# Performance work log

Measured on AMD Instinct MI355X. Metric: run time of the kernel, lower is better.

Reference implementation:

```python
import jax, jax.numpy as jnp
import numpy as np

CUM_P = 0.9  # cumulative_p
MIN_KEEP = 1  # min_tokens_to_keep (<=1 -> branch is a no-op, as in torch default)


def setup_inputs() -> dict:
    key = jax.random.key(0)
    k1, k2 = jax.random.split(key, 2)
    B, D, V = 64, 2048, 50257
    x = jax.random.normal(k1, (B, D), dtype=jnp.float32)
    W = jax.random.normal(k2, (D, V), dtype=jnp.float32) * (1.0 / np.sqrt(D))
    b = jnp.zeros((V,), dtype=jnp.float32)
    return {"x": x, "W": W, "b": b}


def _nucleus_probs(x, W, b):
    # proj + softmax -> probs over vocab  [B, V]
    probs = jax.nn.softmax(x @ W + b, axis=-1)
    # descending sort over vocab
    sorted_idx = jnp.argsort(-probs, axis=-1)                      # [B, V]
    sorted_p = jnp.take_along_axis(probs, sorted_idx, axis=-1)    # [B, V]
    cum = jnp.cumsum(sorted_p, axis=-1)
    remove_sorted = cum > CUM_P
    # shift right by one so the token that crosses the threshold is kept
    remove_sorted = jnp.concatenate(
        [jnp.zeros_like(remove_sorted[..., :1]), remove_sorted[..., :-1]], axis=-1
    )
    # scatter mask back to original vocab order
    rows = jnp.arange(probs.shape[0])[:, None]                     # [B, 1]
    remove = jnp.zeros_like(remove_sorted).at[rows, sorted_idx].set(remove_sorted)
    kept = jnp.where(remove, 0.0, probs)
    # renormalize exactly as torch: p * 1/(sum + 1e-6)
    return kept * (1.0 / (kept.sum(axis=-1, keepdims=True) + 1e-6))


def reference(x, W, b):
    p = _nucleus_probs(x, W, b)                                    # [B, V]
    # Categorical(probs).sample(); zeros -> log = -inf (never sampled)
    return jax.random.categorical(jax.random.key(42), jnp.log(p), axis=-1)
```

## Files before the change

kernel.cpp:

```cpp
#include <hip/hip_runtime.h>
#include <hip/hip_bf16.h>
#include <stdint.h>

#define BB 64
#define DD 2048
#define VV 50257
#define VP 50260
#define NQ 12565
#define NB 4096
#define MAXC 2048
#define QS 8
#define QCH 6283
#define SK 4

typedef __attribute__((ext_vector_type(8))) short short8;
typedef __attribute__((ext_vector_type(4))) float f32x4;
typedef float f32x4u __attribute__((vector_size(16), aligned(4)));

struct U2 { unsigned x, y; };

__device__ __forceinline__ unsigned rotl32(unsigned v, int r) {
  return (v << r) | (v >> (32 - r));
}

__device__ __forceinline__ U2 threefry2x32(unsigned k0, unsigned k1,
                                           unsigned x0, unsigned x1) {
  unsigned k2 = k0 ^ k1 ^ 0x1BD11BDAu;
  x0 += k0; x1 += k1;
#define TF_R4(r1, r2, r3, r4)                         \
  x0 += x1; x1 = rotl32(x1, r1); x1 ^= x0;            \
  x0 += x1; x1 = rotl32(x1, r2); x1 ^= x0;            \
  x0 += x1; x1 = rotl32(x1, r3); x1 ^= x0;            \
  x0 += x1; x1 = rotl32(x1, r4); x1 ^= x0;
  TF_R4(13, 15, 26, 6)   x0 += k1; x1 += k2 + 1u;
  TF_R4(17, 29, 16, 24)  x0 += k2; x1 += k0 + 2u;
  TF_R4(13, 15, 26, 6)   x0 += k0; x1 += k1 + 3u;
  TF_R4(17, 29, 16, 24)  x0 += k1; x1 += k2 + 4u;
  TF_R4(13, 15, 26, 6)   x0 += k2; x1 += k0 + 5u;
#undef TF_R4
  U2 r; r.x = x0; r.y = x1; return r;
}

__device__ __forceinline__ unsigned jax_random_bits(unsigned e) {
  U2 r = threefry2x32(0u, 42u, 0u, e);
  return r.x ^ r.y;
}

__device__ __forceinline__ unsigned mono_key(float zi) {
  unsigned bb = __float_as_uint(zi);
  return bb ^ ((bb >> 31) ? 0xFFFFFFFFu : 0x80000000u);
}

__device__ __forceinline__ unsigned short f2bf_hw(float f) {
  __hip_bfloat16 b = __float2bfloat16(f);
  unsigned short u;
  __builtin_memcpy(&u, &b, 2);
  return u;
}
__device__ __forceinline__ float bf2f(unsigned short h) {
  return __uint_as_float(((unsigned)h) << 16);
}

__global__ __launch_bounds__(256) void pack_x_kernel(
    const float* __restrict__ x, unsigned short* __restrict__ xh,
    unsigned short* __restrict__ xl) {
  int i = blockIdx.x * 256 + threadIdx.x;
  if (i >= 64 * 256) return;
  int b = i >> 8;
  int c = i & 255;
  const float* xp = x + b * 2048 + c * 8;
  short8 hv, lv;
#pragma unroll
  for (int j = 0; j < 8; ++j) {
    float f = xp[j];
    unsigned short h = f2bf_hw(f);
    hv[j] = (short)h;
    lv[j] = (short)f2bf_hw(f - bf2f(h));
  }
  size_t p = ((size_t)c * 64 + b) * 8;
  *(short8*)(xh + p) = hv;
  *(short8*)(xl + p) = lv;
}

__global__ __launch_bounds__(256, 1) void gemm_mfma_kernel(
    const unsigned short* __restrict__ xh, const unsigned short* __restrict__ xl,
    const float* __restrict__ W, float* __restrict__ partial) {
  const int wave = threadIdx.x >> 6;
  const int lane = threadIdx.x & 63;
  const int lo = lane & 15, hi = lane >> 4;
  const int v0w = blockIdx.x * 256 + wave * 64;
  const int vC = v0w + 4 * lo;
  const int ks0 = blockIdx.y * 16;
  const bool edge = (v0w + 64 > VV);

  f32x4 a00 = {0,0,0,0}, a01 = {0,0,0,0}, a02 = {0,0,0,0}, a03 = {0,0,0,0};
  f32x4 a10 = {0,0,0,0}, a11 = {0,0,0,0}, a12 = {0,0,0,0}, a13 = {0,0,0,0};
  f32x4 a20 = {0,0,0,0}, a21 = {0,0,0,0}, a22 = {0,0,0,0}, a23 = {0,0,0,0};
  f32x4 a30 = {0,0,0,0}, a31 = {0,0,0,0}, a32 = {0,0,0,0}, a33 = {0,0,0,0};

  for (int kss = 0; kss < 16; ++kss) {
    const int ks = ks0 + kss;
    const float* wb = W + (size_t)(ks * 32 + hi * 8) * VV;
    f32x4u wq[8];
    if (!edge) {
#pragma unroll
      for (int j = 0; j < 8; ++j)
        wq[j] = *(const f32x4u*)(wb + (size_t)j * VV + vC);
    } else {
#pragma unroll
      for (int j = 0; j < 8; ++j) {
#pragma unroll
        for (int c = 0; c < 4; ++c) {
          int col = vC + c; if (col > VV - 1) col = VV - 1;
          wq[j][c] = wb[(size_t)j * VV + col];
        }
      }
    }
    short8 bh0, bh1, bh2, bh3, bl0, bl1, bl2, bl3;
#pragma unroll
    for (int j = 0; j < 8; ++j) {
      unsigned short h;
      h = f2bf_hw(wq[j][0]); bh0[j] = (short)h; bl0[j] = (short)f2bf_hw(wq[j][0] - bf2f(h));
      h = f2bf_hw(wq[j][1]); bh1[j] = (short)h; bl1[j] = (short)f2bf_hw(wq[j][1] - bf2f(h));
      h = f2bf_hw(wq[j][2]); bh2[j] = (short)h; bl2[j] = (short)f2bf_hw(wq[j][2] - bf2f(h));
      h = f2bf_hw(wq[j][3]); bh3[j] = (short)h; bl3[j] = (short)f2bf_hw(wq[j][3] - bf2f(h));
    }
    const int chunk = ks * 4 + hi;
#define DO_RT(RT, A0, A1, A2, A3)                                           \
    {                                                                       \
      size_t p = ((size_t)chunk * 64 + (RT) * 16 + lo) * 8;                 \
      short8 ah = *(const short8*)(xh + p);                                 \
      short8 al = *(const short8*)(xl + p);                                 \
      A0 = __builtin_amdgcn_mfma_f32_16x16x32_bf16(ah, bh0, A0, 0, 0, 0);   \
      A0 = __builtin_amdgcn_mfma_f32_16x16x32_bf16(al, bh0, A0, 0, 0, 0);   \
      A0 = __builtin_amdgcn_mfma_f32_16x16x32_bf16(ah, bl0, A0, 0, 0, 0);   \
      A1 = __builtin_amdgcn_mfma_f32_16x16x32_bf16(ah, bh1, A1, 0, 0, 0);   \
      A1 = __builtin_amdgcn_mfma_f32_16x16x32_bf16(al, bh1, A1, 0, 0, 0);   \
      A1 = __builtin_amdgcn_mfma_f32_16x16x32_bf16(ah, bl1, A1, 0, 0, 0);   \
      A2 = __builtin_amdgcn_mfma_f32_16x16x32_bf16(ah, bh2, A2, 0, 0, 0);   \
      A2 = __builtin_amdgcn_mfma_f32_16x16x32_bf16(al, bh2, A2, 0, 0, 0);   \
      A2 = __builtin_amdgcn_mfma_f32_16x16x32_bf16(ah, bl2, A2, 0, 0, 0);   \
      A3 = __builtin_amdgcn_mfma_f32_16x16x32_bf16(ah, bh3, A3, 0, 0, 0);   \
      A3 = __builtin_amdgcn_mfma_f32_16x16x32_bf16(al, bh3, A3, 0, 0, 0);   \
      A3 = __builtin_amdgcn_mfma_f32_16x16x32_bf16(ah, bl3, A3, 0, 0, 0);   \
    }
    DO_RT(0, a00, a10, a20, a30)
    DO_RT(1, a01, a11, a21, a31)
    DO_RT(2, a02, a12, a22, a32)
    DO_RT(3, a03, a13, a23, a33)
#undef DO_RT
  }

  float* pp = partial + (size_t)blockIdx.y * BB * VP;
#define ST_RT(RT, A0, A1, A2, A3)                                           \
  {                                                                         \
    _Pragma("unroll")                                                       \
    for (int r = 0; r < 4; ++r) {                                           \
      int row = (RT) * 16 + hi * 4 + r;                                     \
      float4 o; o.x = A0[r]; o.y = A1[r]; o.z = A2[r]; o.w = A3[r];         \
      if (!edge) {                                                          \
        *(float4*)(pp + (size_t)row * VP + vC) = o;                         \
      } else {                                                              \
        if (vC + 0 < VV) pp[(size_t)row * VP + vC + 0] = o.x;               \
        if (vC + 1 < VV) pp[(size_t)row * VP + vC + 1] = o.y;               \
        if (vC + 2 < VV) pp[(size_t)row * VP + vC + 2] = o.z;               \
        if (vC + 3 < VV) pp[(size_t)row * VP + vC + 3] = o.w;               \
      }                                                                     \
    }                                                                       \
  }
  ST_RT(0, a00, a10, a20, a30)
  ST_RT(1, a01, a11, a21, a31)
  ST_RT(2, a02, a12, a22, a32)
  ST_RT(3, a03, a13, a23, a33)
#undef ST_RT
}

__global__ __launch_bounds__(256) void reduce_bias_kernel(
    const float* __restrict__ partial, const float* __restrict__ bias,
    float* __restrict__ logits) {
  int i = blockIdx.x * 256 + threadIdx.x;
  if (i >= BB * NQ) return;
  int b = i / NQ;
  int q = i - b * NQ;
  if (q < NQ - 1) {
    int v = q * 4;
    float4 acc = *(const float4*)(bias + v);
#pragma unroll
    for (int s = 0; s < SK; ++s) {
      float4 p = *(const float4*)(partial + ((size_t)s * BB + b) * VP + v);
      acc.x += p.x; acc.y += p.y; acc.z += p.z; acc.w += p.w;
    }
    *(float4*)(logits + (size_t)b * VP + v) = acc;
  } else {
    int v = VV - 1;
    float acc = bias[v];
#pragma unroll
    for (int s = 0; s < SK; ++s)
      acc += partial[((size_t)s * BB + b) * VP + v];
    logits[(size_t)b * VP + v] = acc;
  }
}

__global__ __launch_bounds__(1024) void nucleus_tstar_kernel(
    const float* __restrict__ logits, unsigned* __restrict__ tstar_out,
    unsigned long long* __restrict__ pack) {
  __shared__ double sd[1024];
  __shared__ float sf[1024];
  __shared__ unsigned su[1024];
  __shared__ double bins[NB];
  __shared__ int cidx[MAXC];
  __shared__ unsigned ckey[MAXC];
  __shared__ double cw[MAXC];
  __shared__ int ccount;
  __shared__ int sh_chunk;
  __shared__ int sh_bstar;
  __shared__ double sh_sabove;

  const int row = blockIdx.x;
  const int tid = threadIdx.x;
  const float* z = logits + (size_t)row * VP;

  for (int i = tid; i < NB; i += 1024) bins[i] = 0.0;
  if (tid == 0) { ccount = 0; sh_chunk = -1; sh_bstar = -1; }
  __syncthreads();

  float mx = -3.4e38f;
  for (int i = tid; i < VV; i += 1024) mx = fmaxf(mx, z[i]);
  sf[tid] = mx; __syncthreads();
  for (int s = 512; s > 0; s >>= 1) {
    if (tid < s) sf[tid] = fmaxf(sf[tid], sf[tid + s]);
    __syncthreads();
  }
  const float m = sf[0];
  __syncthreads();

  for (int i = tid; i < VV; i += 1024) {
    float zi = z[i];
    int bin = (int)((m - zi) * 256.0f);
    bin = (bin < 0) ? 0 : ((bin > NB - 1) ? NB - 1 : bin);
    atomicAdd(&bins[bin], (double)expf(zi - m));
  }
  __syncthreads();

  {
    double c = bins[4 * tid] + bins[4 * tid + 1] + bins[4 * tid + 2] + bins[4 * tid + 3];
    sd[tid] = c; __syncthreads();
    for (int off = 1; off < 1024; off <<= 1) {
      double vv = (tid >= off) ? sd[tid - off] : 0.0;
      __syncthreads();
      sd[tid] += vv;
      __syncthreads();
    }
  }
  const double Z = sd[1023];
  const double C = (double)0.9f * Z;

  if (sd[tid] > C && (tid == 0 || sd[tid - 1] <= C)) sh_chunk = tid;
  __syncthreads();
  if (tid == 0) {
    int tc = sh_chunk;
    if (tc >= 0) {
      double run = (tc > 0) ? sd[tc - 1] : 0.0;
      for (int k = 0; k < 4; ++k) {
        double bw = bins[4 * tc + k];
        if (run + bw > C) { sh_bstar = 4 * tc + k; sh_sabove = run; break; }
        run += bw;
      }
    }
  }
  __syncthreads();
  const int bstar = sh_bstar;
  unsigned tkey = 0u;

  if (bstar >= 0) {
    const double Sab = sh_sabove;
    for (int i = tid; i < VV; i += 1024) {
      float zi = z[i];
      int bin = (int)((m - zi) * 256.0f);
      bin = (bin < 0) ? 0 : ((bin > NB - 1) ? NB - 1 : bin);
      if (bin == bstar) {
        int slot = atomicAdd(&ccount, 1);
        if (slot < MAXC) {
          ckey[slot] = mono_key(zi);
          cidx[slot] = i;
          cw[slot] = (double)expf(zi - m);
        }
      }
    }
    __syncthreads();
    int n = ccount; if (n > MAXC) n = MAXC;
    unsigned mk = 0xFFFFFFFFu;
    for (int i = tid; i < n; i += 1024) {
      unsigned ki = ckey[i]; int ii = cidx[i];
      double T = Sab;
      for (int j = 0; j < n; ++j) {
        unsigned kj = ckey[j];
        if (kj > ki || (kj == ki && cidx[j] < ii)) T += cw[j];
      }
      if (T <= C) mk = (ki < mk) ? ki : mk;
    }
    su[tid] = mk; __syncthreads();
    for (int s = 512; s > 0; s >>= 1) {
      if (tid < s) su[tid] = min(su[tid], su[tid + s]);
      __syncthreads();
    }
    tkey = su[0];
  }
  if (tid == 0) { tstar_out[row] = tkey; pack[row] = 0ull; }
}

__global__ __launch_bounds__(1024) void gumbel_kernel(
    const float* __restrict__ logits, const unsigned* __restrict__ tstar_arr,
    unsigned long long* __restrict__ pack) {
  __shared__ float sf[1024];
  __shared__ int si[1024];
  const int row = blockIdx.x >> 3;
  const int q = blockIdx.x & 7;
  const int tid = threadIdx.x;
  const unsigned tstar = tstar_arr[row];
  const float* z = logits + (size_t)row * VP;
  const int i0 = q * QCH;
  const int i1 = (i0 + QCH < VV) ? (i0 + QCH) : VV;

  float best = -3.4e38f; int bidx = 0x7FFFFFFF;
  for (int i = i0 + tid; i < i1; i += 1024) {
    float zi = z[i];
    if (mono_key(zi) < tstar) continue;
    unsigned e = (unsigned)row * (unsigned)VV + (unsigned)i;
    unsigned bits = jax_random_bits(e);
    float f = __uint_as_float((bits >> 9) | 0x3F800000u) - 1.0f;
    float u = fmaxf(1.17549435082228750797e-38f, f);
    float g = -logf(-logf(u));
    float sc = zi + g;
    if (sc > best) { best = sc; bidx = i; }
  }
  sf[tid] = best; si[tid] = bidx; __syncthreads();
  for (int s = 512; s > 0; s >>= 1) {
    if (tid < s) {
      float ob = sf[tid + s]; int oi = si[tid + s];
      if (ob > sf[tid] || (ob == sf[tid] && oi < si[tid])) {
        sf[tid] = ob; si[tid] = oi;
      }
    }
    __syncthreads();
  }
  if (tid == 0 && si[0] != 0x7FFFFFFF) {
    unsigned long long p = ((unsigned long long)mono_key(sf[0]) << 32) |
                           (unsigned long long)(0xFFFFFFFFu - (unsigned)si[0]);
    atomicMax(pack + row, p);
  }
}

__global__ __launch_bounds__(64) void unpack_kernel(
    const unsigned long long* __restrict__ pack, int* __restrict__ out) {
  int r = threadIdx.x;
  if (r < BB) out[r] = (int)(0xFFFFFFFFu - (unsigned)(pack[r] & 0xFFFFFFFFull));
}

extern "C" void kernel_launch(void* const* d_in, const int* in_sizes, int n_in,
                              void* d_out, int out_size, void* d_ws, size_t ws_size,
                              hipStream_t stream) {
  const float* x = (const float*)d_in[0];
  const float* W = (const float*)d_in[1];
  const float* bias = (const float*)d_in[2];
  int* out = (int*)d_out;
  char* ws = (char*)d_ws;

  unsigned short* xh = (unsigned short*)ws;
  unsigned short* xl = (unsigned short*)(ws + 262144);
  float* logits = (float*)(ws + 524288);
  float* partial = (float*)(ws + 13390848);
  unsigned* tstar = (unsigned*)(ws + 64857088);
  unsigned long long* pack = (unsigned long long*)(ws + 64857344);

  pack_x_kernel<<<64, 256, 0, stream>>>(x, xh, xl);
  const int cblocks = (VV + 255) / 256;
  dim3 g(cblocks, SK);
  gemm_mfma_kernel<<<g, 256, 0, stream>>>(xh, xl, W, partial);
  reduce_bias_kernel<<<(BB * NQ + 255) / 256, 256, 0, stream>>>(
      partial, bias, logits);
  nucleus_tstar_kernel<<<BB, 1024, 0, stream>>>(logits, tstar, pack);
  gumbel_kernel<<<BB * QS, 1024, 0, stream>>>(logits, tstar, pack);
  unpack_kernel<<<1, 64, 0, stream>>>(pack, out);
}
```

Measured before the change: 182.0 us.

## Fuse split-K reduction and bias into GEMM via in-block LDS accumulation

The split-K factor of 4 now lives inside each block: the four waves handle different K quarters of the same 64-column tile instead of four blocks along grid y. The waves sum their partial tiles in shared memory one after another, then the block adds the bias and writes logits directly. This drops the separate reduce kernel and the roughly 51 MB round trip of partial sums through global memory. In exchange there are four times more blocks, each covering a narrow 64-column slice, plus serialized LDS accumulation with four barriers.

```diff
diff --git a/kernel.cpp b/kernel.cpp
--- a/kernel.cpp
+++ b/kernel.cpp
@@ -6,12 +6,10 @@
 #define DD 2048
 #define VV 50257
 #define VP 50260
-#define NQ 12565
 #define NB 4096
 #define MAXC 2048
 #define QS 8
 #define QCH 6283
-#define SK 4
 
 typedef __attribute__((ext_vector_type(8))) short short8;
 typedef __attribute__((ext_vector_type(4))) float f32x4;
@@ -84,14 +82,16 @@
 
 __global__ __launch_bounds__(256, 1) void gemm_mfma_kernel(
     const unsigned short* __restrict__ xh, const unsigned short* __restrict__ xl,
-    const float* __restrict__ W, float* __restrict__ partial) {
+    const float* __restrict__ W, const float* __restrict__ bias,
+    float* __restrict__ logits) {
+  __shared__ float lacc[64][68];
   const int wave = threadIdx.x >> 6;
   const int lane = threadIdx.x & 63;
   const int lo = lane & 15, hi = lane >> 4;
-  const int v0w = blockIdx.x * 256 + wave * 64;
-  const int vC = v0w + 4 * lo;
-  const int ks0 = blockIdx.y * 16;
-  const bool edge = (v0w + 64 > VV);
+  const int v0blk = blockIdx.x * 64;
+  const int vC = v0blk + 4 * lo;
+  const int ks0 = wave * 16;
+  const bool edge = (v0blk + 64 > VV);
 
   f32x4 a00 = {0,0,0,0}, a01 = {0,0,0,0}, a02 = {0,0,0,0}, a03 = {0,0,0,0};
   f32x4 a10 = {0,0,0,0}, a11 = {0,0,0,0}, a12 = {0,0,0,0}, a13 = {0,0,0,0};
@@ -151,53 +151,51 @@
 #undef DO_RT
   }
 
-  float* pp = partial + (size_t)blockIdx.y * BB * VP;
-#define ST_RT(RT, A0, A1, A2, A3)                                           \
+#define LACC_RT(RT, A0, A1, A2, A3, FIRST)                                  \
   {                                                                         \
     _Pragma("unroll")                                                       \
     for (int r = 0; r < 4; ++r) {                                           \
       int row = (RT) * 16 + hi * 4 + r;                                     \
-      float4 o; o.x = A0[r]; o.y = A1[r]; o.z = A2[r]; o.w = A3[r];         \
-      if (!edge) {                                                          \
-        *(float4*)(pp + (size_t)row * VP + vC) = o;                         \
-      } else {                                                              \
-        if (vC + 0 < VV) pp[(size_t)row * VP + vC + 0] = o.x;               \
-        if (vC + 1 < VV) pp[(size_t)row * VP + vC + 1] = o.y;               \
-        if (vC + 2 < VV) pp[(size_t)row * VP + vC + 2] = o.z;               \
-        if (vC + 3 < VV) pp[(size_t)row * VP + vC + 3] = o.w;               \
-      }                                                                     \
+      float* p = &lacc[row][4 * lo];                                        \
+      if (FIRST) { p[0] = A0[r]; p[1] = A1[r]; p[2] = A2[r]; p[3] = A3[r]; }\
+      else { p[0] += A0[r]; p[1] += A1[r]; p[2] += A2[r]; p[3] += A3[r]; }  \
     }                                                                       \
   }
-  ST_RT(0, a00, a10, a20, a30)
-  ST_RT(1, a01, a11, a21, a31)
-  ST_RT(2, a02, a12, a22, a32)
-  ST_RT(3, a03, a13, a23, a33)
-#undef ST_RT
-}
-
-__global__ __launch_bounds__(256) void reduce_bias_kernel(
-    const float* __restrict__ partial, const float* __restrict__ bias,
-    float* __restrict__ logits) {
-  int i = blockIdx.x * 256 + threadIdx.x;
-  if (i >= BB * NQ) return;
-  int b = i / NQ;
-  int q = i - b * NQ;
-  if (q < NQ - 1) {
-    int v = q * 4;
-    float4 acc = *(const float4*)(bias + v);
-#pragma unroll
-    for (int s = 0; s < SK; ++s) {
-      float4 p = *(const float4*)(partial + ((size_t)s * BB + b) * VP + v);
-      acc.x += p.x; acc.y += p.y; acc.z += p.z; acc.w += p.w;
-    }
-    *(float4*)(logits + (size_t)b * VP + v) = acc;
-  } else {
-    int v = VV - 1;
-    float acc = bias[v];
-#pragma unroll
-    for (int s = 0; s < SK; ++s)
-      acc += partial[((size_t)s * BB + b) * VP + v];
-    logits[(size_t)b * VP + v] = acc;
+  for (int w = 0; w < 4; ++w) {
+    if (wave == w) {
+      if (w == 0) {
+        LACC_RT(0, a00, a10, a20, a30, true)
+        LACC_RT(1, a01, a11, a21, a31, true)
+        LACC_RT(2, a02, a12, a22, a32, true)
+        LACC_RT(3, a03, a13, a23, a33, true)
+      } else {
+        LACC_RT(0, a00, a10, a20, a30, false)
+        LACC_RT(1, a01, a11, a21, a31, false)
+        LACC_RT(2, a02, a12, a22, a32, false)
+        LACC_RT(3, a03, a13, a23, a33, false)
+      }
+    }
+    __syncthreads();
+  }
+#undef LACC_RT
+
+#pragma unroll
+  for (int k = 0; k < 4; ++k) {
+    int q = (int)threadIdx.x + k * 256;
+    int row = q >> 4;
+    int c4 = (q & 15) * 4;
+    int col = v0blk + c4;
+    float4 s = *(float4*)&lacc[row][c4];
+    if (!edge) {
+      float4 bv = *(const float4*)(bias + col);
+      s.x += bv.x; s.y += bv.y; s.z += bv.z; s.w += bv.w;
+      *(float4*)(logits + (size_t)row * VP + col) = s;
+    } else {
+      if (col + 0 < VV) logits[(size_t)row * VP + col + 0] = s.x + bias[col + 0];
+      if (col + 1 < VV) logits[(size_t)row * VP + col + 1] = s.y + bias[col + 1];
+      if (col + 2 < VV) logits[(size_t)row * VP + col + 2] = s.z + bias[col + 2];
+      if (col + 3 < VV) logits[(size_t)row * VP + col + 3] = s.w + bias[col + 3];
+    }
   }
 }
 
@@ -369,16 +367,12 @@
   unsigned short* xh = (unsigned short*)ws;
   unsigned short* xl = (unsigned short*)(ws + 262144);
   float* logits = (float*)(ws + 524288);
-  float* partial = (float*)(ws + 13390848);
-  unsigned* tstar = (unsigned*)(ws + 64857088);
-  unsigned long long* pack = (unsigned long long*)(ws + 64857344);
+  unsigned* tstar = (unsigned*)(ws + 13390848);
+  unsigned long long* pack = (unsigned long long*)(ws + 13391104);
 
   pack_x_kernel<<<64, 256, 0, stream>>>(x, xh, xl);
-  const int cblocks = (VV + 255) / 256;
-  dim3 g(cblocks, SK);
-  gemm_mfma_kernel<<<g, 256, 0, stream>>>(xh, xl, W, partial);
-  reduce_bias_kernel<<<(BB * NQ + 255) / 256, 256, 0, stream>>>(
-      partial, bias, logits);
+  const int cblocks = (VV + 63) / 64;
+  gemm_mfma_kernel<<<cblocks, 256, 0, stream>>>(xh, xl, W, bias, logits);
   nucleus_tstar_kernel<<<BB, 1024, 0, stream>>>(logits, tstar, pack);
   gumbel_kernel<<<BB * QS, 1024, 0, stream>>>(logits, tstar, pack);
   unpack_kernel<<<1, 64, 0, stream>>>(pack, out);
```

Result: no change. 181.0 us (-0.6%).
